# Optimization experiments

Measured on AMD Instinct MI355X. Metric: run time of the kernel, lower is better.

The kernel has to match this reference:

```python
import jax, jax.numpy as jnp
import numpy as np

T = 16384  # total training steps (length of LR schedule)
M = 8192   # number of evaluated checkpoints
HUBER_DELTA = 0.001


def _huber(delta, r):
    a = jnp.abs(r)
    return jnp.where(a <= delta, 0.5 * r * r, delta * (a - 0.5 * delta))


def setup_inputs() -> dict:
    key = jax.random.key(0)
    k1, k2, k3 = jax.random.split(key, 3)
    # realistic positive LR schedule (~3e-4), required since lrs**(-gamma) is taken
    lrs = jax.random.uniform(k1, (T,), dtype=jnp.float32) * 3e-4 + 1e-5
    lr_sum = jnp.cumsum(lrs)
    step = jnp.sort(jax.random.randint(k2, (M,), 0, T))
    S1 = lr_sum[step]  # cumulative LR sum at the evaluated steps
    # lr_gap = consecutive LR differences (delta of the schedule); index 0 unused
    lr_gap = jnp.concatenate([jnp.zeros((1,), jnp.float32), lrs[:-1] - lrs[1:]])
    loss = jax.random.uniform(k3, (M,), dtype=jnp.float32) + 2.0  # positive (log taken)
    p = lambda v: jnp.float32(v)
    return {
        "S1": S1, "lrs": lrs, "lr_sum": lr_sum, "step": step,
        "lr_gap": lr_gap, "loss": loss,
        "L0": p(2.5), "A": p(0.5), "alpha": p(0.5), "B": p(300.0),
        "C": p(1.0), "beta": p(0.5), "gamma": p(0.6),
    }


def reference(S1, lrs, lr_sum, step, lr_gap, loss, L0, A, alpha, B, C, beta, gamma):
    # Vectorized triangular reduction replacing the per-step Python loop:
    # for step s: LD = sum_{k=1..s} lr_gap[k] * (1 - (1 + C*lrs[k]^-gamma*(lr_sum[s]-lr_sum[k-1]))^-beta)
    Tn = lrs.shape[0]
    k = jnp.arange(Tn)
    mask = (k[None, :] >= 1) & (k[None, :] <= step[:, None])  # [M, T]
    lr_sum_prev = jnp.concatenate([jnp.zeros((1,), lr_sum.dtype), lr_sum[:-1]])
    G = lr_sum[step][:, None] - lr_sum_prev[None, :]          # lr_sum[s] - lr_sum[k-1]
    G = jnp.where(mask, G, 0.0)                               # keep base positive where masked
    inner = 1.0 + C * (lrs ** (-gamma))[None, :] * G          # [M, T]
    term = lr_gap[None, :] * (1.0 - inner ** (-beta))
    LD = jnp.sum(jnp.where(mask, term, 0.0), axis=1)          # [M]
    pred = L0 + A * S1 ** (-alpha) + B * LD
    r = jnp.log(loss) - jnp.log(jnp.clip(pred, 1e-10))
    return _huber(HUBER_DELTA, r).sum()
```

## Files before the change

### kernel.cpp

```cpp
#include <hip/hip_runtime.h>
#include <math.h>

#define GSZ 8
#define PAD 4

#if __has_builtin(__builtin_amdgcn_rsqf)
#define RSQF(x) __builtin_amdgcn_rsqf(x)
#else
#define RSQF(x) (1.0f / sqrtf(x))
#endif

__global__ __launch_bounds__(256) void precompute_kernel(
    const float* __restrict__ lrs, const float* __restrict__ lr_sum,
    const float* __restrict__ lr_gap,
    float* __restrict__ cpw, float* __restrict__ dd, float* __restrict__ gapp,
    const float* __restrict__ gamma_p, const float* __restrict__ C_p, int T) {
  int i = blockIdx.x * 256 + threadIdx.x;
  if (i >= T + PAD) return;
  if (i == 0 || i >= T) {
    cpw[i] = 0.0f; dd[i] = 1.0f; gapp[i] = 0.0f;
    return;
  }
  float c = C_p[0] * powf(lrs[i], -gamma_p[0]);
  cpw[i]  = c;
  dd[i]   = fmaf(-c, lr_sum[i - 1], 1.0f);
  gapp[i] = lr_gap[i];
}

template <bool USE_RSQ>
__device__ __forceinline__ void ld_body(
    const float* __restrict__ cpw, const float* __restrict__ dd,
    const float* __restrict__ gapp,
    const float (&Ss)[GSZ], const int (&sv)[GSZ], float (&acc)[GSZ],
    int kEnd1, int smax, float nb) {
  int tid = threadIdx.x;

  for (int k0 = tid * 4; k0 < kEnd1; k0 += 1024) {
    float4 c4 = *(const float4*)(cpw + k0);
    float4 d4 = *(const float4*)(dd + k0);
    float4 g4 = *(const float4*)(gapp + k0);
    const float ce[4] = {c4.x, c4.y, c4.z, c4.w};
    const float de[4] = {d4.x, d4.y, d4.z, d4.w};
    const float ge[4] = {g4.x, g4.y, g4.z, g4.w};
#pragma unroll
    for (int e = 0; e < 4; ++e) {
#pragma unroll
      for (int j = 0; j < GSZ; ++j) {
        float inner = fmaf(ce[e], Ss[j], de[e]);
        float p = USE_RSQ ? RSQF(inner) : __expf(nb * __logf(inner));
        acc[j] = fmaf(ge[e], p, acc[j]);
      }
    }
  }

  for (int k0 = kEnd1 + tid * 4; k0 <= smax; k0 += 1024) {
    float4 c4 = *(const float4*)(cpw + k0);
    float4 d4 = *(const float4*)(dd + k0);
    float4 g4 = *(const float4*)(gapp + k0);
    const float ce[4] = {c4.x, c4.y, c4.z, c4.w};
    const float de[4] = {d4.x, d4.y, d4.z, d4.w};
    const float ge[4] = {g4.x, g4.y, g4.z, g4.w};
#pragma unroll
    for (int e = 0; e < 4; ++e) {
#pragma unroll
      for (int j = 0; j < GSZ; ++j) {
        float inner = fmaf(ce[e], Ss[j], de[e]);
        float p = USE_RSQ ? RSQF(inner) : __expf(nb * __logf(inner));
        float pm = (k0 + e <= sv[j]) ? p : 0.0f;
        acc[j] = fmaf(ge[e], pm, acc[j]);
      }
    }
  }
}

__global__ __launch_bounds__(256) void ld_kernel(
    const float* __restrict__ S1, const int* __restrict__ step,
    const float* __restrict__ loss, const float* __restrict__ lrs,
    const float* __restrict__ cpw, const float* __restrict__ dd,
    const float* __restrict__ gapp,
    const float* __restrict__ L0_p, const float* __restrict__ A_p,
    const float* __restrict__ alpha_p, const float* __restrict__ B_p,
    const float* __restrict__ beta_p,
    float* __restrict__ hub, int M) {
  int mbase = blockIdx.x * GSZ;

  float Ss[GSZ]; int sv[GSZ]; float acc[GSZ];
#pragma unroll
  for (int j = 0; j < GSZ; ++j) {
    int m = mbase + j;
    Ss[j] = S1[m];
    sv[j] = step[m];
    acc[j] = 0.0f;
  }
  int smin = sv[0], smax = sv[0];
#pragma unroll
  for (int j = 1; j < GSZ; ++j) {
    smin = min(smin, sv[j]);
    smax = max(smax, sv[j]);
  }
  int kEnd1 = ((smin + 1) >> 10) << 10;

  float beta = beta_p[0];
  float nb = -beta;
  if (beta == 0.5f)
    ld_body<true>(cpw, dd, gapp, Ss, sv, acc, kEnd1, smax, nb);
  else
    ld_body<false>(cpw, dd, gapp, Ss, sv, acc, kEnd1, smax, nb);

  __shared__ float wacc[4][GSZ];
  int lane = threadIdx.x & 63, wid = threadIdx.x >> 6;
#pragma unroll
  for (int j = 0; j < GSZ; ++j) {
    float v = acc[j];
#pragma unroll
    for (int off = 32; off; off >>= 1) v += __shfl_down(v, off, 64);
    if (lane == 0) wacc[wid][j] = v;
  }
  __syncthreads();

  if (threadIdx.x < GSZ) {
    int j = threadIdx.x;
    int m = mbase + j;
    float sgp = wacc[0][j] + wacc[1][j] + wacc[2][j] + wacc[3][j];
    int s = step[m];
    float Ssum = S1[m];
    float LD = (lrs[0] - lrs[s]) - sgp;
    float pred = L0_p[0] + A_p[0] * powf(Ssum, -alpha_p[0]) + B_p[0] * LD;
    pred = fmaxf(pred, 1e-10f);
    float r = logf(loss[m]) - logf(pred);
    float a = fabsf(r);
    const float dlt = 0.001f;
    hub[m] = (a <= dlt) ? (0.5f * r * r) : (dlt * (a - 0.5f * dlt));
  }
}

__global__ __launch_bounds__(1024) void reduce_kernel(
    const float* __restrict__ hub, float* __restrict__ out, int M) {
  float acc = 0.0f;
  for (int i = threadIdx.x; i < M; i += 1024) acc += hub[i];
#pragma unroll
  for (int off = 32; off; off >>= 1) acc += __shfl_down(acc, off, 64);
  __shared__ float wacc[16];
  int lane = threadIdx.x & 63, wid = threadIdx.x >> 6;
  if (lane == 0) wacc[wid] = acc;
  __syncthreads();
  if (threadIdx.x == 0) {
    float t = 0.0f;
#pragma unroll
    for (int i = 0; i < 16; ++i) t += wacc[i];
    out[0] = t;
  }
}

extern "C" void kernel_launch(void* const* d_in, const int* in_sizes, int n_in,
                              void* d_out, int out_size, void* d_ws, size_t ws_size,
                              hipStream_t stream) {
  const float* S1      = (const float*)d_in[0];
  const float* lrs     = (const float*)d_in[1];
  const float* lr_sum  = (const float*)d_in[2];
  const int*   step    = (const int*)  d_in[3];
  const float* lr_gap  = (const float*)d_in[4];
  const float* loss    = (const float*)d_in[5];
  const float* L0_p    = (const float*)d_in[6];
  const float* A_p     = (const float*)d_in[7];
  const float* alpha_p = (const float*)d_in[8];
  const float* B_p     = (const float*)d_in[9];
  const float* C_p     = (const float*)d_in[10];
  const float* beta_p  = (const float*)d_in[11];
  const float* gamma_p = (const float*)d_in[12];

  int M = in_sizes[0];
  int T = in_sizes[1];
  int Tp = T + PAD;

  float* cpw  = (float*)d_ws;
  float* dd   = cpw + Tp;
  float* gapp = dd + Tp;
  float* hub  = gapp + Tp;

  precompute_kernel<<<(Tp + 255) / 256, 256, 0, stream>>>(
      lrs, lr_sum, lr_gap, cpw, dd, gapp, gamma_p, C_p, T);
  ld_kernel<<<M / GSZ, 256, 0, stream>>>(
      S1, step, loss, lrs, cpw, dd, gapp,
      L0_p, A_p, alpha_p, B_p, beta_p, hub, M);
  reduce_kernel<<<1, 1024, 0, stream>>>(hub, (float*)d_out, M);
}
```

Before: 27.75 us.

## Pair triangular chunks per block and widen blocks to 512 threads

After: 27.37 us. About the same (-1.4%).

```diff
diff --git a/kernel.cpp b/kernel.cpp
--- a/kernel.cpp
+++ b/kernel.cpp
@@ -1,14 +1,20 @@
 #include <hip/hip_runtime.h>
 #include <math.h>
 
+#define BLK 512
 #define GSZ 8
 #define PAD 4
+#define KSTRIDE (BLK*4)
 
 #if __has_builtin(__builtin_amdgcn_rsqf)
 #define RSQF(x) __builtin_amdgcn_rsqf(x)
 #else
 #define RSQF(x) (1.0f / sqrtf(x))
 #endif
+
+__device__ __forceinline__ float fast_pow(float x, float e) {
+  return __expf(e * __logf(x));
+}
 
 __global__ __launch_bounds__(256) void precompute_kernel(
     const float* __restrict__ lrs, const float* __restrict__ lr_sum,
@@ -21,7 +27,7 @@
     cpw[i] = 0.0f; dd[i] = 1.0f; gapp[i] = 0.0f;
     return;
   }
-  float c = C_p[0] * powf(lrs[i], -gamma_p[0]);
+  float c = C_p[0] * fast_pow(lrs[i], -gamma_p[0]);
   cpw[i]  = c;
   dd[i]   = fmaf(-c, lr_sum[i - 1], 1.0f);
   gapp[i] = lr_gap[i];
@@ -35,7 +41,7 @@
     int kEnd1, int smax, float nb) {
   int tid = threadIdx.x;
 
-  for (int k0 = tid * 4; k0 < kEnd1; k0 += 1024) {
+  for (int k0 = tid * 4; k0 < kEnd1; k0 += KSTRIDE) {
     float4 c4 = *(const float4*)(cpw + k0);
     float4 d4 = *(const float4*)(dd + k0);
     float4 g4 = *(const float4*)(gapp + k0);
@@ -53,7 +59,7 @@
     }
   }
 
-  for (int k0 = kEnd1 + tid * 4; k0 <= smax; k0 += 1024) {
+  for (int k0 = kEnd1 + tid * 4; k0 <= smax; k0 += KSTRIDE) {
     float4 c4 = *(const float4*)(cpw + k0);
     float4 d4 = *(const float4*)(dd + k0);
     float4 g4 = *(const float4*)(gapp + k0);
@@ -73,7 +79,64 @@
   }
 }
 
-__global__ __launch_bounds__(256) void ld_kernel(
+template <bool USE_RSQ>
+__device__ __forceinline__ void process_chunk(
+    int chunk,
+    const float* __restrict__ S1, const int* __restrict__ step,
+    const float* __restrict__ loss, const float* __restrict__ lrs,
+    const float* __restrict__ cpw, const float* __restrict__ dd,
+    const float* __restrict__ gapp,
+    float L0, float A, float alpha, float B, float nb,
+    float (&wacc)[BLK / 64][GSZ], float* __restrict__ hub) {
+  int mbase = chunk * GSZ;
+
+  float Ss[GSZ]; int sv[GSZ]; float acc[GSZ];
+#pragma unroll
+  for (int j = 0; j < GSZ; ++j) {
+    Ss[j] = S1[mbase + j];
+    sv[j] = step[mbase + j];
+    acc[j] = 0.0f;
+  }
+  int smin = sv[0], smax = sv[0];
+#pragma unroll
+  for (int j = 1; j < GSZ; ++j) {
+    smin = min(smin, sv[j]);
+    smax = max(smax, sv[j]);
+  }
+  int kEnd1 = ((smin + 1) / KSTRIDE) * KSTRIDE;
+
+  ld_body<USE_RSQ>(cpw, dd, gapp, Ss, sv, acc, kEnd1, smax, nb);
+
+  int lane = threadIdx.x & 63, wid = threadIdx.x >> 6;
+#pragma unroll
+  for (int j = 0; j < GSZ; ++j) {
+    float v = acc[j];
+#pragma unroll
+    for (int off = 32; off; off >>= 1) v += __shfl_down(v, off, 64);
+    if (lane == 0) wacc[wid][j] = v;
+  }
+  __syncthreads();
+
+  if (threadIdx.x < GSZ) {
+    int j = threadIdx.x;
+    int m = mbase + j;
+    float sgp = 0.0f;
+#pragma unroll
+    for (int w = 0; w < BLK / 64; ++w) sgp += wacc[w][j];
+    int s = step[m];
+    float Ssum = S1[m];
+    float LD = (lrs[0] - lrs[s]) - sgp;
+    float pred = L0 + A * fast_pow(Ssum, -alpha) + B * LD;
+    pred = fmaxf(pred, 1e-10f);
+    float r = __logf(loss[m]) - __logf(pred);
+    float a = fabsf(r);
+    const float dlt = 0.001f;
+    hub[m] = (a <= dlt) ? (0.5f * r * r) : (dlt * (a - 0.5f * dlt));
+  }
+  __syncthreads();
+}
+
+__global__ __launch_bounds__(BLK, 4) void ld_kernel(
     const float* __restrict__ S1, const int* __restrict__ step,
     const float* __restrict__ loss, const float* __restrict__ lrs,
     const float* __restrict__ cpw, const float* __restrict__ dd,
@@ -81,56 +144,28 @@
     const float* __restrict__ L0_p, const float* __restrict__ A_p,
     const float* __restrict__ alpha_p, const float* __restrict__ B_p,
     const float* __restrict__ beta_p,
-    float* __restrict__ hub, int M) {
-  int mbase = blockIdx.x * GSZ;
-
-  float Ss[GSZ]; int sv[GSZ]; float acc[GSZ];
-#pragma unroll
-  for (int j = 0; j < GSZ; ++j) {
-    int m = mbase + j;
-    Ss[j] = S1[m];
-    sv[j] = step[m];
-    acc[j] = 0.0f;
-  }
-  int smin = sv[0], smax = sv[0];
-#pragma unroll
-  for (int j = 1; j < GSZ; ++j) {
-    smin = min(smin, sv[j]);
-    smax = max(smax, sv[j]);
-  }
-  int kEnd1 = ((smin + 1) >> 10) << 10;
-
+    float* __restrict__ hub, int nchunk) {
+  __shared__ float wacc[BLK / 64][GSZ];
+
+  float L0 = L0_p[0], A = A_p[0], alpha = alpha_p[0], B = B_p[0];
   float beta = beta_p[0];
   float nb = -beta;
-  if (beta == 0.5f)
-    ld_body<true>(cpw, dd, gapp, Ss, sv, acc, kEnd1, smax, nb);
-  else
-    ld_body<false>(cpw, dd, gapp, Ss, sv, acc, kEnd1, smax, nb);
-
-  __shared__ float wacc[4][GSZ];
-  int lane = threadIdx.x & 63, wid = threadIdx.x >> 6;
-#pragma unroll
-  for (int j = 0; j < GSZ; ++j) {
-    float v = acc[j];
-#pragma unroll
-    for (int off = 32; off; off >>= 1) v += __shfl_down(v, off, 64);
-    if (lane == 0) wacc[wid][j] = v;
-  }
-  __syncthreads();
-
-  if (threadIdx.x < GSZ) {
-    int j = threadIdx.x;
-    int m = mbase + j;
-    float sgp = wacc[0][j] + wacc[1][j] + wacc[2][j] + wacc[3][j];
-    int s = step[m];
-    float Ssum = S1[m];
-    float LD = (lrs[0] - lrs[s]) - sgp;
-    float pred = L0_p[0] + A_p[0] * powf(Ssum, -alpha_p[0]) + B_p[0] * LD;
-    pred = fmaxf(pred, 1e-10f);
-    float r = logf(loss[m]) - logf(pred);
-    float a = fabsf(r);
-    const float dlt = 0.001f;
-    hub[m] = (a <= dlt) ? (0.5f * r * r) : (dlt * (a - 0.5f * dlt));
+
+  int c0 = blockIdx.x;
+  int c1 = nchunk - 1 - c0;
+
+  if (beta == 0.5f) {
+    process_chunk<true>(c0, S1, step, loss, lrs, cpw, dd, gapp,
+                        L0, A, alpha, B, nb, wacc, hub);
+    if (c1 != c0)
+      process_chunk<true>(c1, S1, step, loss, lrs, cpw, dd, gapp,
+                          L0, A, alpha, B, nb, wacc, hub);
+  } else {
+    process_chunk<false>(c0, S1, step, loss, lrs, cpw, dd, gapp,
+                         L0, A, alpha, B, nb, wacc, hub);
+    if (c1 != c0)
+      process_chunk<false>(c1, S1, step, loss, lrs, cpw, dd, gapp,
+                           L0, A, alpha, B, nb, wacc, hub);
   }
 }
 
@@ -178,10 +213,13 @@
   float* gapp = dd + Tp;
   float* hub  = gapp + Tp;
 
+  int nchunk = M / GSZ;
+  int nblocks = (nchunk + 1) / 2;
+
   precompute_kernel<<<(Tp + 255) / 256, 256, 0, stream>>>(
       lrs, lr_sum, lr_gap, cpw, dd, gapp, gamma_p, C_p, T);
-  ld_kernel<<<M / GSZ, 256, 0, stream>>>(
+  ld_kernel<<<nblocks, BLK, 0, stream>>>(
       S1, step, loss, lrs, cpw, dd, gapp,
-      L0_p, A_p, alpha_p, B_p, beta_p, hub, M);
+      L0_p, A_p, alpha_p, B_p, beta_p, hub, nchunk);
   reduce_kernel<<<1, 1024, 0, stream>>>(hub, (float*)d_out, M);
 }
```
